# Kernel optimization log

Hardware: AMD Instinct MI355X
Metric: run time of the kernel (lower is better)

Reference implementation:

```python
import jax, jax.numpy as jnp
import numpy as np

EPS = 1e-5


def _shift1d(x, s, axis):
    """out[..., y, ...] = linear interp of x at position y + s along `axis`,
    zero-padded outside (== grid_sample bilinear, padding_mode='zeros',
    align_corners=True, for a pure axis-aligned shift of s pixels)."""
    n = x.shape[axis]
    f = jnp.floor(s)
    frac = (s - f).astype(x.dtype)  # scalar in [0,1)
    fi = f.astype(jnp.int32)

    def gather(off):
        idx = jnp.arange(n) + fi + off
        mask = (idx >= 0) & (idx < n)
        v = jnp.take(x, jnp.clip(idx, 0, n - 1), axis=axis)
        mshape = [1] * x.ndim
        mshape[axis] = n
        return v * mask.reshape(mshape).astype(x.dtype)

    return (1 - frac) * gather(0) + frac * gather(1)


def _axial_dw(x, w_h, w_w, r):
    """ContinuousAxialDW: x + depthwise learnable-dilation conv along H and W.
    w_h, w_w: (C, k) per-channel taps."""
    r = jnp.maximum(r, 1.0)
    c = x.shape[1]
    kh = w_h.shape[1]
    kw = w_w.shape[1]
    acc_h = jnp.zeros_like(x)
    for i, off in enumerate(range(-(kh // 2), kh // 2 + 1)):
        acc_h = acc_h + _shift1d(x, off * r, 2) * w_h[:, i].reshape(1, c, 1, 1)
    acc_w = jnp.zeros_like(x)
    for i, off in enumerate(range(-(kw // 2), kw // 2 + 1)):
        acc_w = acc_w + _shift1d(x, off * r, 3) * w_w[:, i].reshape(1, c, 1, 1)
    return x + acc_h + acc_w


def _bn(x, g, b, m, v):
    sh = (1, -1, 1, 1)
    scale = g.reshape(sh) * jax.lax.rsqrt(v.reshape(sh) + EPS)
    return (x - m.reshape(sh)) * scale + b.reshape(sh)


def _prelu(x, a):
    return jnp.where(x >= 0, x, a.reshape(1, -1, 1, 1) * x)


def _pw(w, x):  # 1x1 conv, no bias. w: (O, C)
    return jnp.einsum('oc,bchw->bohw', w, x)


def _dwconv3(x, w, axis):  # depthwise 3-tap conv, 'same' zero padding. w: (C, 3)
    c = x.shape[1]
    n = x.shape[axis]
    pad = [(0, 0)] * 4
    pad[axis] = (1, 1)
    xp = jnp.pad(x, pad)
    out = jnp.zeros_like(x)
    for i in range(3):
        out = out + jax.lax.slice_in_dim(xp, i, i + n, axis=axis) * w[:, i].reshape(1, c, 1, 1)
    return out


def _coord_att(x, w1, bn1, a1, wh, ww):
    n, c, h, w = x.shape
    xh = x.mean(axis=3, keepdims=True)                     # (n,c,h,1)
    xw = jnp.transpose(x.mean(axis=2, keepdims=True), (0, 1, 3, 2))  # (n,c,w,1)
    y = jnp.concatenate([xh, xw], axis=2)                  # (n,c,h+w,1)
    y = _prelu(_bn(_pw(w1, y), *bn1), a1)                  # (n,mip,h+w,1)
    yh, yw = y[:, :, :h], jnp.transpose(y[:, :, h:], (0, 1, 3, 2))
    a_h = jax.nn.sigmoid(_pw(wh, yh))                      # (n,c,h,1)
    a_w = jax.nn.sigmoid(_pw(ww, yw))                      # (n,c,1,w)
    return x * a_w * a_h


def _forward(x, r_m, wh_m, ww_m, r_l, wh_l, ww_l, w_fuse,
             bnf_g, bnf_b, bnf_m, bnf_v,
             dg_wh, dg_ww, dg_g, dg_b, dg_m, dg_v, act_a,
             ca_w1, ca_g, ca_b, ca_m, ca_v, ca_a, ca_wh, ca_ww):
    m = _axial_dw(x, wh_m, ww_m, r_m)
    l = _axial_dw(x, wh_l, ww_l, r_l)
    fused = _bn(_pw(w_fuse, m + l), bnf_g, bnf_b, bnf_m, bnf_v)
    edges = _dwconv3(x, dg_wh, 2) + _dwconv3(x, dg_ww, 3)
    anchor = _bn(x + edges, dg_g, dg_b, dg_m, dg_v)
    out = _prelu(fused + anchor, act_a)
    return _coord_att(out, ca_w1, (ca_g, ca_b, ca_m, ca_v), ca_a, ca_wh, ca_ww)


def setup_inputs() -> dict:
    key = jax.random.key(0)
    ks = jax.random.split(key, 16)
    B, C, H, W = 8, 96, 128, 128
    K = 5      # mixer kernel taps
    MIP = 8    # max(8, C // 32)

    def rn(k, shape, scale=1.0):
        return jax.random.normal(k, shape, dtype=jnp.float32) * scale

    f32 = jnp.float32
    return {
        'x': rn(ks[0], (B, C, H, W)),
        'r_m': jnp.array(4.0, f32),
        'wh_m': rn(ks[1], (C, K), 0.2), 'ww_m': rn(ks[2], (C, K), 0.2),
        'r_l': jnp.array(8.0, f32),
        'wh_l': rn(ks[3], (C, K), 0.2), 'ww_l': rn(ks[4], (C, K), 0.2),
        'w_fuse': rn(ks[5], (C, C), 0.1),
        'bnf_g': jnp.ones((C,), f32), 'bnf_b': jnp.zeros((C,), f32),
        'bnf_m': jnp.zeros((C,), f32), 'bnf_v': jnp.ones((C,), f32),
        'dg_wh': rn(ks[6], (C, 3), 0.3), 'dg_ww': rn(ks[7], (C, 3), 0.3),
        'dg_g': jnp.ones((C,), f32), 'dg_b': jnp.zeros((C,), f32),
        'dg_m': jnp.zeros((C,), f32), 'dg_v': jnp.ones((C,), f32),
        'act_a': jnp.full((C,), 0.25, f32),
        'ca_w1': rn(ks[8], (MIP, C), 0.1),
        'ca_g': jnp.ones((MIP,), f32), 'ca_b': jnp.zeros((MIP,), f32),
        'ca_m': jnp.zeros((MIP,), f32), 'ca_v': jnp.ones((MIP,), f32),
        'ca_a': jnp.full((MIP,), 0.25, f32),
        'ca_wh': rn(ks[9], (C, MIP), 0.3),
        'ca_ww': rn(ks[10], (C, MIP), 0.3),
    }


def reference(x, r_m, wh_m, ww_m, r_l, wh_l, ww_l, w_fuse,
              bnf_g, bnf_b, bnf_m, bnf_v,
              dg_wh, dg_ww, dg_g, dg_b, dg_m, dg_v, act_a,
              ca_w1, ca_g, ca_b, ca_m, ca_v, ca_a, ca_wh, ca_ww):
    return _forward(x, r_m, wh_m, ww_m, r_l, wh_l, ww_l, w_fuse,
                    bnf_g, bnf_b, bnf_m, bnf_v,
                    dg_wh, dg_ww, dg_g, dg_b, dg_m, dg_v, act_a,
                    ca_w1, ca_g, ca_b, ca_m, ca_v, ca_a, ca_wh, ca_ww)
```

## Files before the change

kernel.cpp:

```cpp
#include <hip/hip_runtime.h>
#include <hip/hip_bf16.h>
#include <math.h>

#define Bn 8
#define Cn 96
#define Hn 128
#define Wn 128
#define PLANE (Hn*Wn)
#define NIMG (Bn*Cn*PLANE)
#define EPSV 1e-5f
#define TAPN 48
#define TAPF 8

typedef __attribute__((ext_vector_type(8))) short short8;
typedef __attribute__((ext_vector_type(4))) float floatx4;

union FragU { short8 v; uint2 u2[2]; };

__global__ __launch_bounds__(256) void k0_taps(
    const float* __restrict__ rm_p, const float* __restrict__ whm, const float* __restrict__ wwm,
    const float* __restrict__ rl_p, const float* __restrict__ whl, const float* __restrict__ wwl,
    int* __restrict__ cnt, int* __restrict__ offs, float* __restrict__ wts)
{
    __shared__ float dense[2 * Cn][TAPN + 1];

    int t = threadIdx.x;
    for (int e = t; e < 2 * Cn * (TAPN + 1); e += 256)
        ((float*)dense)[e] = 0.f;
    __syncthreads();

    if (t >= Cn * 2) return;
    int c = t >> 1, dir = t & 1;
    const float* tap_m = dir ? (wwm + c * 5) : (whm + c * 5);
    const float* tap_l = dir ? (wwl + c * 5) : (whl + c * 5);
    float rm = fmaxf(rm_p[0], 1.f), rl = fmaxf(rl_p[0], 1.f);
    for (int pass = 0; pass < 2; ++pass) {
        float r = pass ? rl : rm;
        const float* tp = pass ? tap_l : tap_m;
        for (int i = 0; i < 5; ++i) {
            float s = (float)(i - 2) * r;
            float f = floorf(s);
            float fr = s - f;
            int fi = (int)f + 23;
            if (fi >= 0 && fi < TAPN)         dense[t][fi]     += tp[i] * (1.f - fr);
            if (fi + 1 >= 0 && fi + 1 < TAPN) dense[t][fi + 1] += tp[i] * fr;
        }
    }
    int n = 0;
    int*   orow = offs + t * TAPN;
    float* wrow = wts  + t * TAPN;
    for (int k = 0; k < TAPN; ++k) {
        float wv = dense[t][k];
        if (wv != 0.f) { orow[n] = k - 23; wrow[n] = wv; ++n; }
    }
    cnt[t] = n;
    for (int k = n; k < TAPN; ++k) { orow[k] = 0; wrow[k] = 0.f; }
}

__global__ __launch_bounds__(512) void k1_axial(
    const float* __restrict__ x,
    const int* __restrict__ cnt, const int* __restrict__ offs, const float* __restrict__ wts,
    const float* __restrict__ dwh, const float* __restrict__ dww,
    const float* __restrict__ dg, const float* __restrict__ db_,
    const float* __restrict__ dm, const float* __restrict__ dv,
    short* __restrict__ t_bf, float* __restrict__ anchor,
    float* __restrict__ xw_zero)
{
    __shared__ float pl[Hn][160];

    int bc  = blockIdx.x;
    int b   = bc / Cn;
    int c   = bc % Cn;
    int tid = threadIdx.x;

    if (tid < Wn) xw_zero[bc * Wn + tid] = 0.f;

    const float* plane = x + ((long)bc << 14);

    const float4* p4 = (const float4*)plane;
#pragma unroll
    for (int it = 0; it < 8; ++it) {
        int idx = tid + it * 512;
        int r = idx >> 5, c4 = idx & 31;
        *(float4*)&pl[r][16 + c4 * 4] = p4[idx];
    }
#pragma unroll
    for (int it = 0; it < 2; ++it) {
        int idx = tid + it * 512;
        int r = idx >> 3, pq = idx & 7;
        int col = (pq < 4) ? pq * 4 : 144 + (pq - 4) * 4;
        *(float4*)&pl[r][col] = (float4){0.f, 0.f, 0.f, 0.f};
    }

    int cH = cnt[c * 2], cW = cnt[c * 2 + 1];
    int soH[TAPF], soW[TAPF];
    float swH[TAPF], swW[TAPF];
#pragma unroll
    for (int j = 0; j < TAPF; ++j) {
        soH[j] = offs[(c * 2) * TAPN + j];
        swH[j] = wts[(c * 2) * TAPN + j];
        soW[j] = offs[(c * 2 + 1) * TAPN + j];
        swW[j] = wts[(c * 2 + 1) * TAPN + j];
    }
    bool fast = (cH <= TAPF) && (cW <= TAPF);
#pragma unroll
    for (int j = 0; j < TAPF; ++j)
        fast = fast && (soW[j] >= -16) && (soW[j] <= 16);

    float e0 = dwh[c * 3], e1 = dwh[c * 3 + 1], e2 = dwh[c * 3 + 2];
    float f0 = dww[c * 3], f1 = dww[c * 3 + 1], f2 = dww[c * 3 + 2];
    float dsc = dg[c] * rsqrtf(dv[c] + EPSV);
    float dof = db_[c] - dm[c] * dsc;

    __syncthreads();

    int m      = tid & 31;
    int rowgrp = tid >> 5;
    short* tbase = t_bf + ((long)(b * Hn) * Cn + c) * Wn;
    float* abase = anchor + ((long)bc << 14);

    for (int k = 0; k < 8; ++k) {
        int h = k * 16 + rowgrp;
        float vc0 = pl[h][16 + m];
        float vc1 = pl[h][16 + m + 32];
        float vc2 = pl[h][16 + m + 64];
        float vc3 = pl[h][16 + m + 96];
        float a0 = 2.f * vc0, a1 = 2.f * vc1, a2 = 2.f * vc2, a3 = 2.f * vc3;

        if (fast) {
#pragma unroll
            for (int j = 0; j < TAPF; ++j) {
                int y = h + soH[j];
                float wt = (y >= 0 && y < Hn) ? swH[j] : 0.f;
                y = min(max(y, 0), Hn - 1);
                a0 += wt * pl[y][16 + m];
                a1 += wt * pl[y][16 + m + 32];
                a2 += wt * pl[y][16 + m + 64];
                a3 += wt * pl[y][16 + m + 96];
            }
#pragma unroll
            for (int j = 0; j < TAPF; ++j) {
                int o = soW[j];
                float wt = swW[j];
                a0 += wt * pl[h][16 + m + o];
                a1 += wt * pl[h][16 + m + 32 + o];
                a2 += wt * pl[h][16 + m + 64 + o];
                a3 += wt * pl[h][16 + m + 96 + o];
            }
        } else {
            const int*   goH = offs + (c * 2 + 0) * TAPN;
            const float* gwH = wts  + (c * 2 + 0) * TAPN;
            const int*   goW = offs + (c * 2 + 1) * TAPN;
            const float* gwW = wts  + (c * 2 + 1) * TAPN;
            for (int j = 0; j < cH; ++j) {
                int y = h + goH[j];
                if (y >= 0 && y < Hn) {
                    float wt = gwH[j];
                    const float* rp = plane + (y << 7);
                    a0 += wt * rp[m];
                    a1 += wt * rp[m + 32];
                    a2 += wt * rp[m + 64];
                    a3 += wt * rp[m + 96];
                }
            }
            for (int j = 0; j < cW; ++j) {
                int o = goW[j];
                float wt = gwW[j];
                const float* rp = plane + (h << 7);
#pragma unroll
                for (int q = 0; q < 4; ++q) {
                    int xw = m + 32 * q + o;
                    float v = (xw >= 0 && xw < Wn) ? rp[xw] : 0.f;
                    float* ap = (q == 0) ? &a0 : (q == 1) ? &a1 : (q == 2) ? &a2 : &a3;
                    *ap += wt * v;
                }
            }
        }

        short* tp = tbase + (long)h * (Cn * Wn);
        {
            __hip_bfloat16 h0 = __float2bfloat16(a0), h1 = __float2bfloat16(a1);
            __hip_bfloat16 h2 = __float2bfloat16(a2), h3 = __float2bfloat16(a3);
            tp[m]      = *(short*)&h0;
            tp[m + 32] = *(short*)&h1;
            tp[m + 64] = *(short*)&h2;
            tp[m + 96] = *(short*)&h3;
        }

        int yu = (h > 0) ? h - 1 : 0;
        int yd = (h < Hn - 1) ? h + 1 : Hn - 1;
        float wu = (h > 0) ? e0 : 0.f;
        float wd = (h < Hn - 1) ? e2 : 0.f;
        float* ap = abase + (h << 7);
#pragma unroll
        for (int q = 0; q < 4; ++q) {
            int col = 16 + m + 32 * q;
            float vcq = (q == 0) ? vc0 : (q == 1) ? vc1 : (q == 2) ? vc2 : vc3;
            float vu = pl[yu][col];
            float vd = pl[yd][col];
            float vl = pl[h][col - 1];
            float vr = pl[h][col + 1];
            float edges = wu * vu + e1 * vcq + wd * vd + f0 * vl + f1 * vcq + f2 * vr;
            ap[m + 32 * q] = (vcq + edges) * dsc + dof;
        }
    }
}

__global__ __launch_bounds__(256) void k2_pw(
    const short* __restrict__ t_bf, const float* __restrict__ anchor,
    const float* __restrict__ w_fuse,
    const float* __restrict__ bg, const float* __restrict__ bb,
    const float* __restrict__ bm, const float* __restrict__ bv,
    const float* __restrict__ act_a,
    float* __restrict__ out)
{
    __shared__ short wl[Cn * 100];
    __shared__ short tl[64 * 100];
    __shared__ float sfsc[Cn], sfof[Cn], saa[Cn];

    int tid  = threadIdx.x;
    int blk  = blockIdx.x;
    int b    = blk >> 8;
    int r    = blk & 255;
    int h    = r >> 1;
    int hb   = r & 1;
    int lane = tid & 63;
    int wv   = tid >> 6;
    int n16  = lane & 15;
    int quad = lane >> 4;

    {
        uint* wdst = (uint*)wl;
        for (int e = tid; e < Cn * 48; e += 256) {
            int o = e / 48, cq = e - o * 48;
            float f0 = w_fuse[o * Cn + 2 * cq];
            float f1 = w_fuse[o * Cn + 2 * cq + 1];
            __hip_bfloat16 h0 = __float2bfloat16(f0);
            __hip_bfloat16 h1 = __float2bfloat16(f1);
            uint u = (uint)(*(unsigned short*)&h0) |
                     ((uint)(*(unsigned short*)&h1) << 16);
            wdst[o * 50 + cq] = u;
        }
    }
    if (tid < Cn) {
        float s = bg[tid] * rsqrtf(bv[tid] + EPSV);
        sfsc[tid] = s;
        sfof[tid] = bb[tid] - bm[tid] * s;
        saa[tid]  = act_a[tid];
    }
    {
        const uint* trow = (const uint*)t_bf + (size_t)(b * Hn + h) * Cn * 64 + hb * 32;
#pragma unroll
        for (int rep = 0; rep < 3; ++rep) {
            int task = tid + rep * 256;
            int cg = task >> 5, j = task & 31;
            int c0 = cg * 4;
            uint v0 = trow[(c0 + 0) * 64 + j];
            uint v1 = trow[(c0 + 1) * 64 + j];
            uint v2 = trow[(c0 + 2) * 64 + j];
            uint v3 = trow[(c0 + 3) * 64 + j];
            uint2 lo, hi;
            lo.x = (v0 & 0xffffu) | (v1 << 16);
            lo.y = (v2 & 0xffffu) | (v3 << 16);
            hi.x = (v0 >> 16) | (v1 & 0xffff0000u);
            hi.y = (v2 >> 16) | (v3 & 0xffff0000u);
            *(uint2*)(tl + (2 * j) * 100 + c0)     = lo;
            *(uint2*)(tl + (2 * j + 1) * 100 + c0) = hi;
        }
    }
    __syncthreads();

    FragU Bf[3];
    {
        int p = wv * 16 + n16;
        const short* bp = tl + p * 100 + quad * 8;
#pragma unroll
        for (int kb = 0; kb < 3; ++kb) {
            Bf[kb].u2[0] = *(const uint2*)(bp + kb * 32);
            Bf[kb].u2[1] = *(const uint2*)(bp + kb * 32 + 4);
        }
    }

    floatx4 acc[6];
#pragma unroll
    for (int mt = 0; mt < 6; ++mt)
        acc[mt] = (floatx4){0.f, 0.f, 0.f, 0.f};

#pragma unroll
    for (int mt = 0; mt < 6; ++mt) {
        int o = mt * 16 + n16;
        const short* apg = wl + o * 100 + quad * 8;
        FragU Af[3];
#pragma unroll
        for (int kb = 0; kb < 3; ++kb) {
            Af[kb].u2[0] = *(const uint2*)(apg + kb * 32);
            Af[kb].u2[1] = *(const uint2*)(apg + kb * 32 + 4);
        }
#pragma unroll
        for (int kb = 0; kb < 3; ++kb)
            acc[mt] = __builtin_amdgcn_mfma_f32_16x16x32_bf16(
                Af[kb].v, Bf[kb].v, acc[mt], 0, 0, 0);
    }

    long base = (long)b * Cn * PLANE + (h << 7) + hb * 64;
    int p = wv * 16 + n16;
#pragma unroll
    for (int mt = 0; mt < 6; ++mt) {
#pragma unroll
        for (int reg = 0; reg < 4; ++reg) {
            int o = mt * 16 + quad * 4 + reg;
            long idx = base + (long)o * PLANE + p;
            float fused = acc[mt][reg] * sfsc[o] + sfof[o];
            float v = fused + anchor[idx];
            out[idx] = (v >= 0.f) ? v : saa[o] * v;
        }
    }
}

__global__ __launch_bounds__(256) void k3_means(
    const float* __restrict__ op, float* __restrict__ xh, float* __restrict__ xw)
{
    int blk = blockIdx.x;
    int bc  = blk >> 2;
    int q   = blk & 3;
    const float4* pl = (const float4*)(op + ((long)bc << 14) + (q << 12));
    int tid = threadIdx.x;
    int wq = tid & 31;
    int hg = tid >> 5;
    __shared__ float cpart[8][Wn + 4];
    __shared__ float rpart[32];
    float4 csum = make_float4(0, 0, 0, 0);
#pragma unroll
    for (int k = 0; k < 4; ++k) {
        int hl = hg * 4 + k;
        float4 v = pl[hl * 32 + wq];
        csum.x += v.x; csum.y += v.y; csum.z += v.z; csum.w += v.w;
        float rs = v.x + v.y + v.z + v.w;
#pragma unroll
        for (int off = 16; off; off >>= 1) rs += __shfl_down(rs, off, 32);
        if (wq == 0) rpart[hl] = rs * (1.f / Wn);
    }
    cpart[hg][wq * 4 + 0] = csum.x;
    cpart[hg][wq * 4 + 1] = csum.y;
    cpart[hg][wq * 4 + 2] = csum.z;
    cpart[hg][wq * 4 + 3] = csum.w;
    __syncthreads();
    if (tid < 128) {
        float s = 0.f;
#pragma unroll
        for (int g = 0; g < 8; ++g) s += cpart[g][tid];
        atomicAdd(&xw[bc * Wn + tid], s);
    }
    if (tid < 32) xh[bc * Hn + q * 32 + tid] = rpart[tid];
}

__global__ __launch_bounds__(256) void kf_att_scale(
    const float* __restrict__ xh, const float* __restrict__ xw,
    const float* __restrict__ w1,
    const float* __restrict__ g, const float* __restrict__ bb,
    const float* __restrict__ m, const float* __restrict__ v,
    const float* __restrict__ aa,
    const float* __restrict__ cwh, const float* __restrict__ cww,
    float* __restrict__ out)
{
    __shared__ float w1s[8 * Cn];
    __shared__ float sah[Hn];
    __shared__ float saw[Wn];

    int bc  = blockIdx.x;
    int b   = bc / Cn;
    int c   = bc % Cn;
    int p   = threadIdx.x;

    for (int e = p; e < 8 * Cn; e += 256) w1s[e] = w1[e];
    __syncthreads();

    bool isH = (p < Hn);
    const float* src = isH ? (xh + ((long)b * Cn) * Hn + p)
                           : (xw + ((long)b * Cn) * Wn + (p - Hn));
    float scale = isH ? 1.f : (1.f / Hn);

    float acc[8];
#pragma unroll
    for (int i = 0; i < 8; ++i) acc[i] = 0.f;
    for (int cc = 0; cc < Cn; ++cc) {
        float yv = src[(long)cc * Hn] * scale;
#pragma unroll
        for (int mip = 0; mip < 8; ++mip) acc[mip] += w1s[mip * Cn + cc] * yv;
    }
    const float* wsel = isH ? (cwh + c * 8) : (cww + c * 8);
    float s = 0.f;
#pragma unroll
    for (int mip = 0; mip < 8; ++mip) {
        float sc = g[mip] * rsqrtf(v[mip] + EPSV);
        float t = (acc[mip] - m[mip]) * sc + bb[mip];
        float yv = (t >= 0.f) ? t : aa[mip] * t;
        s += wsel[mip] * yv;
    }
    float av = 1.f / (1.f + expf(-s));
    if (isH) sah[p] = av; else saw[p - Hn] = av;
    __syncthreads();

    float4* p4 = (float4*)(out + ((long)bc << 14));
#pragma unroll
    for (int it = 0; it < 16; ++it) {
        int idx = p + it * 256;
        int h = idx >> 5;
        int w4 = idx & 31;
        float4 vv = p4[idx];
        float ah = sah[h];
        float4 aw = *(float4*)&saw[w4 * 4];
        float4 r;
        r.x = vv.x * ah * aw.x;
        r.y = vv.y * ah * aw.y;
        r.z = vv.z * ah * aw.z;
        r.w = vv.w * ah * aw.w;
        p4[idx] = r;
    }
}

extern "C" void kernel_launch(void* const* d_in, const int* in_sizes, int n_in,
                              void* d_out, int out_size, void* d_ws, size_t ws_size,
                              hipStream_t stream)
{
    const float* x     = (const float*)d_in[0];
    const float* r_m   = (const float*)d_in[1];
    const float* wh_m  = (const float*)d_in[2];
    const float* ww_m  = (const float*)d_in[3];
    const float* r_l   = (const float*)d_in[4];
    const float* wh_l  = (const float*)d_in[5];
    const float* ww_l  = (const float*)d_in[6];
    const float* wfuse = (const float*)d_in[7];
    const float* bnf_g = (const float*)d_in[8];
    const float* bnf_b = (const float*)d_in[9];
    const float* bnf_m = (const float*)d_in[10];
    const float* bnf_v = (const float*)d_in[11];
    const float* dg_wh = (const float*)d_in[12];
    const float* dg_ww = (const float*)d_in[13];
    const float* dg_g  = (const float*)d_in[14];
    const float* dg_b  = (const float*)d_in[15];
    const float* dg_m  = (const float*)d_in[16];
    const float* dg_v  = (const float*)d_in[17];
    const float* act_a = (const float*)d_in[18];
    const float* ca_w1 = (const float*)d_in[19];
    const float* ca_g  = (const float*)d_in[20];
    const float* ca_b  = (const float*)d_in[21];
    const float* ca_m  = (const float*)d_in[22];
    const float* ca_v  = (const float*)d_in[23];
    const float* ca_a  = (const float*)d_in[24];
    const float* ca_wh = (const float*)d_in[25];
    const float* ca_ww = (const float*)d_in[26];

    float* ws     = (float*)d_ws;
    float* anchor = ws;
    float* xh     = anchor + (size_t)NIMG;
    float* xw     = xh + Bn * Cn * Hn;
    float* wts    = xw + Bn * Cn * Wn;
    int*   cnt    = (int*)(wts + 2 * Cn * TAPN);
    int*   offs   = cnt + 2 * Cn;
    short* t_bf   = (short*)(offs + 2 * Cn * TAPN);

    float* out = (float*)d_out;

    hipLaunchKernelGGL(k0_taps, dim3(1), dim3(256), 0, stream,
                       r_m, wh_m, ww_m, r_l, wh_l, ww_l, cnt, offs, wts);
    hipLaunchKernelGGL(k1_axial, dim3(Bn * Cn), dim3(512), 0, stream,
                       x, cnt, offs, wts, dg_wh, dg_ww, dg_g, dg_b, dg_m, dg_v,
                       t_bf, anchor, xw);
    hipLaunchKernelGGL(k2_pw, dim3(Bn * Hn * 2), dim3(256), 0, stream,
                       t_bf, anchor, wfuse, bnf_g, bnf_b, bnf_m, bnf_v, act_a, out);
    hipLaunchKernelGGL(k3_means, dim3(Bn * Cn * 4), dim3(256), 0, stream,
                       out, xh, xw);
    hipLaunchKernelGGL(kf_att_scale, dim3(Bn * Cn), dim3(256), 0, stream,
                       xh, xw, ca_w1, ca_g, ca_b, ca_m, ca_v, ca_a, ca_wh, ca_ww,
                       out);
}
```

Baseline: 229.1 us.

## Split axial kernel into half-plane blocks, pre-convert fuse weights, prefetch anchor

The axial depthwise kernel now handles half an image plane per block, with a 16-row halo loaded into a smaller shared tile. This doubles the grid and cuts shared memory per block to improve occupancy, at the cost of redundant halo loads. The fast path now also requires vertical offsets within the halo; larger offsets fall back to the global-memory path. The 1x1-conv weights are converted to bf16 once in the setup kernel instead of in every pointwise block, and the anchor loads are issued before the MFMA section to hide their latency.

```diff
diff --git a/kernel.cpp b/kernel.cpp
--- a/kernel.cpp
+++ b/kernel.cpp
@@ -20,11 +20,17 @@
 __global__ __launch_bounds__(256) void k0_taps(
     const float* __restrict__ rm_p, const float* __restrict__ whm, const float* __restrict__ wwm,
     const float* __restrict__ rl_p, const float* __restrict__ whl, const float* __restrict__ wwl,
-    int* __restrict__ cnt, int* __restrict__ offs, float* __restrict__ wts)
+    const float* __restrict__ w_fuse,
+    int* __restrict__ cnt, int* __restrict__ offs, float* __restrict__ wts,
+    short* __restrict__ w_bf)
 {
     __shared__ float dense[2 * Cn][TAPN + 1];
 
     int t = threadIdx.x;
+    for (int e = t; e < Cn * Cn; e += 256) {
+        __hip_bfloat16 hv = __float2bfloat16(w_fuse[e]);
+        w_bf[e] = *(short*)&hv;
+    }
     for (int e = t; e < 2 * Cn * (TAPN + 1); e += 256)
         ((float*)dense)[e] = 0.f;
     __syncthreads();
@@ -66,30 +72,37 @@
     short* __restrict__ t_bf, float* __restrict__ anchor,
     float* __restrict__ xw_zero)
 {
-    __shared__ float pl[Hn][160];
-
-    int bc  = blockIdx.x;
-    int b   = bc / Cn;
-    int c   = bc % Cn;
-    int tid = threadIdx.x;
-
-    if (tid < Wn) xw_zero[bc * Wn + tid] = 0.f;
+    __shared__ float pl[96][160];
+
+    int blk  = blockIdx.x;
+    int bc   = blk >> 1;
+    int half = blk & 1;
+    int r0   = half << 6;
+    int b    = bc / Cn;
+    int c    = bc % Cn;
+    int tid  = threadIdx.x;
+
+    if (half == 0 && tid < Wn) xw_zero[bc * Wn + tid] = 0.f;
 
     const float* plane = x + ((long)bc << 14);
 
     const float4* p4 = (const float4*)plane;
 #pragma unroll
-    for (int it = 0; it < 8; ++it) {
+    for (int it = 0; it < 6; ++it) {
         int idx = tid + it * 512;
-        int r = idx >> 5, c4 = idx & 31;
-        *(float4*)&pl[r][16 + c4 * 4] = p4[idx];
+        int lr = idx >> 5, c4 = idx & 31;
+        int y = r0 - 16 + lr;
+        if (y >= 0 && y < Hn)
+            *(float4*)&pl[lr][16 + c4 * 4] = p4[y * 32 + c4];
     }
 #pragma unroll
     for (int it = 0; it < 2; ++it) {
         int idx = tid + it * 512;
-        int r = idx >> 3, pq = idx & 7;
-        int col = (pq < 4) ? pq * 4 : 144 + (pq - 4) * 4;
-        *(float4*)&pl[r][col] = (float4){0.f, 0.f, 0.f, 0.f};
+        if (idx < 768) {
+            int lr = idx >> 3, pq = idx & 7;
+            int col = (pq < 4) ? pq * 4 : 144 + (pq - 4) * 4;
+            *(float4*)&pl[lr][col] = (float4){0.f, 0.f, 0.f, 0.f};
+        }
     }
 
     int cH = cnt[c * 2], cW = cnt[c * 2 + 1];
@@ -104,8 +117,10 @@
     }
     bool fast = (cH <= TAPF) && (cW <= TAPF);
 #pragma unroll
-    for (int j = 0; j < TAPF; ++j)
+    for (int j = 0; j < TAPF; ++j) {
         fast = fast && (soW[j] >= -16) && (soW[j] <= 16);
+        fast = fast && (soH[j] >= -16) && (soH[j] <= 16);
+    }
 
     float e0 = dwh[c * 3], e1 = dwh[c * 3 + 1], e2 = dwh[c * 3 + 2];
     float f0 = dww[c * 3], f1 = dww[c * 3 + 1], f2 = dww[c * 3 + 2];
@@ -119,12 +134,14 @@
     short* tbase = t_bf + ((long)(b * Hn) * Cn + c) * Wn;
     float* abase = anchor + ((long)bc << 14);
 
-    for (int k = 0; k < 8; ++k) {
-        int h = k * 16 + rowgrp;
-        float vc0 = pl[h][16 + m];
-        float vc1 = pl[h][16 + m + 32];
-        float vc2 = pl[h][16 + m + 64];
-        float vc3 = pl[h][16 + m + 96];
+    for (int k = 0; k < 4; ++k) {
+        int hl = k * 16 + rowgrp;
+        int h  = r0 + hl;
+        int lc = hl + 16;
+        float vc0 = pl[lc][16 + m];
+        float vc1 = pl[lc][16 + m + 32];
+        float vc2 = pl[lc][16 + m + 64];
+        float vc3 = pl[lc][16 + m + 96];
         float a0 = 2.f * vc0, a1 = 2.f * vc1, a2 = 2.f * vc2, a3 = 2.f * vc3;
 
         if (fast) {
@@ -133,19 +150,20 @@
                 int y = h + soH[j];
                 float wt = (y >= 0 && y < Hn) ? swH[j] : 0.f;
                 y = min(max(y, 0), Hn - 1);
-                a0 += wt * pl[y][16 + m];
-                a1 += wt * pl[y][16 + m + 32];
-                a2 += wt * pl[y][16 + m + 64];
-                a3 += wt * pl[y][16 + m + 96];
+                int ly = y - r0 + 16;
+                a0 += wt * pl[ly][16 + m];
+                a1 += wt * pl[ly][16 + m + 32];
+                a2 += wt * pl[ly][16 + m + 64];
+                a3 += wt * pl[ly][16 + m + 96];
             }
 #pragma unroll
             for (int j = 0; j < TAPF; ++j) {
                 int o = soW[j];
                 float wt = swW[j];
-                a0 += wt * pl[h][16 + m + o];
-                a1 += wt * pl[h][16 + m + 32 + o];
-                a2 += wt * pl[h][16 + m + 64 + o];
-                a3 += wt * pl[h][16 + m + 96 + o];
+                a0 += wt * pl[lc][16 + m + o];
+                a1 += wt * pl[lc][16 + m + 32 + o];
+                a2 += wt * pl[lc][16 + m + 64 + o];
+                a3 += wt * pl[lc][16 + m + 96 + o];
             }
         } else {
             const int*   goH = offs + (c * 2 + 0) * TAPN;
@@ -189,6 +207,8 @@
 
         int yu = (h > 0) ? h - 1 : 0;
         int yd = (h < Hn - 1) ? h + 1 : Hn - 1;
+        int lyu = yu - r0 + 16;
+        int lyd = yd - r0 + 16;
         float wu = (h > 0) ? e0 : 0.f;
         float wd = (h < Hn - 1) ? e2 : 0.f;
         float* ap = abase + (h << 7);
@@ -196,10 +216,10 @@
         for (int q = 0; q < 4; ++q) {
             int col = 16 + m + 32 * q;
             float vcq = (q == 0) ? vc0 : (q == 1) ? vc1 : (q == 2) ? vc2 : vc3;
-            float vu = pl[yu][col];
-            float vd = pl[yd][col];
-            float vl = pl[h][col - 1];
-            float vr = pl[h][col + 1];
+            float vu = pl[lyu][col];
+            float vd = pl[lyd][col];
+            float vl = pl[lc][col - 1];
+            float vr = pl[lc][col + 1];
             float edges = wu * vu + e1 * vcq + wd * vd + f0 * vl + f1 * vcq + f2 * vr;
             ap[m + 32 * q] = (vcq + edges) * dsc + dof;
         }
@@ -208,7 +228,7 @@
 
 __global__ __launch_bounds__(256) void k2_pw(
     const short* __restrict__ t_bf, const float* __restrict__ anchor,
-    const float* __restrict__ w_fuse,
+    const short* __restrict__ w_bf,
     const float* __restrict__ bg, const float* __restrict__ bb,
     const float* __restrict__ bm, const float* __restrict__ bv,
     const float* __restrict__ act_a,
@@ -230,16 +250,11 @@
     int quad = lane >> 4;
 
     {
+        const uint* wsrc = (const uint*)w_bf;
         uint* wdst = (uint*)wl;
         for (int e = tid; e < Cn * 48; e += 256) {
             int o = e / 48, cq = e - o * 48;
-            float f0 = w_fuse[o * Cn + 2 * cq];
-            float f1 = w_fuse[o * Cn + 2 * cq + 1];
-            __hip_bfloat16 h0 = __float2bfloat16(f0);
-            __hip_bfloat16 h1 = __float2bfloat16(f1);
-            uint u = (uint)(*(unsigned short*)&h0) |
-                     ((uint)(*(unsigned short*)&h1) << 16);
-            wdst[o * 50 + cq] = u;
+            wdst[o * 50 + cq] = wsrc[e];
         }
     }
     if (tid < Cn) {
@@ -268,11 +283,22 @@
             *(uint2*)(tl + (2 * j + 1) * 100 + c0) = hi;
         }
     }
+
+    long base = (long)b * Cn * PLANE + (h << 7) + hb * 64;
+    int p = wv * 16 + n16;
+    float anc[6][4];
+#pragma unroll
+    for (int mt = 0; mt < 6; ++mt)
+#pragma unroll
+        for (int reg = 0; reg < 4; ++reg) {
+            int o = mt * 16 + quad * 4 + reg;
+            anc[mt][reg] = anchor[base + (long)o * PLANE + p];
+        }
+
     __syncthreads();
 
     FragU Bf[3];
     {
-        int p = wv * 16 + n16;
         const short* bp = tl + p * 100 + quad * 8;
 #pragma unroll
         for (int kb = 0; kb < 3; ++kb) {
@@ -302,8 +328,6 @@
                 Af[kb].v, Bf[kb].v, acc[mt], 0, 0, 0);
     }
 
-    long base = (long)b * Cn * PLANE + (h << 7) + hb * 64;
-    int p = wv * 16 + n16;
 #pragma unroll
     for (int mt = 0; mt < 6; ++mt) {
 #pragma unroll
@@ -311,7 +335,7 @@
             int o = mt * 16 + quad * 4 + reg;
             long idx = base + (long)o * PLANE + p;
             float fused = acc[mt][reg] * sfsc[o] + sfof[o];
-            float v = fused + anchor[idx];
+            float v = fused + anc[mt][reg];
             out[idx] = (v >= 0.f) ? v : saa[o] * v;
         }
     }
@@ -459,16 +483,18 @@
     int*   cnt    = (int*)(wts + 2 * Cn * TAPN);
     int*   offs   = cnt + 2 * Cn;
     short* t_bf   = (short*)(offs + 2 * Cn * TAPN);
+    short* w_bf   = t_bf + (size_t)NIMG;
 
     float* out = (float*)d_out;
 
     hipLaunchKernelGGL(k0_taps, dim3(1), dim3(256), 0, stream,
-                       r_m, wh_m, ww_m, r_l, wh_l, ww_l, cnt, offs, wts);
-    hipLaunchKernelGGL(k1_axial, dim3(Bn * Cn), dim3(512), 0, stream,
+                       r_m, wh_m, ww_m, r_l, wh_l, ww_l, wfuse,
+                       cnt, offs, wts, w_bf);
+    hipLaunchKernelGGL(k1_axial, dim3(Bn * Cn * 2), dim3(512), 0, stream,
                        x, cnt, offs, wts, dg_wh, dg_ww, dg_g, dg_b, dg_m, dg_v,
                        t_bf, anchor, xw);
     hipLaunchKernelGGL(k2_pw, dim3(Bn * Hn * 2), dim3(256), 0, stream,
-                       t_bf, anchor, wfuse, bnf_g, bnf_b, bnf_m, bnf_v, act_a, out);
+                       t_bf, anchor, w_bf, bnf_g, bnf_b, bnf_m, bnf_v, act_a, out);
     hipLaunchKernelGGL(k3_means, dim3(Bn * Cn * 4), dim3(256), 0, stream,
                        out, xh, xw);
     hipLaunchKernelGGL(kf_att_scale, dim3(Bn * Cn), dim3(256), 0, stream,
```

After: 229.2 us. Within noise of the previous version (+0.0%).
